# Performance work log

Measured on AMD Instinct MI355X. Metric: run time of the kernel, lower is better.

Reference implementation:

```python
import jax, jax.numpy as jnp
import numpy as np
import math

S, B, D = 2048, 8, 256
HEADS = 8
DPROJ = 128
DFF = 1024
DH = DPROJ // HEADS  # 16


def _layernorm(x, g, b, eps=1e-5):
    mu = jnp.mean(x, axis=-1, keepdims=True)
    var = jnp.mean((x - mu) ** 2, axis=-1, keepdims=True)
    return (x - mu) * jax.lax.rsqrt(var + eps) * g + b


def setup_inputs() -> dict:
    key = jax.random.key(0)
    ks = jax.random.split(key, 16)
    s = 0.02
    return {
        "src": jax.random.normal(ks[0], (S, B, D), dtype=jnp.float32),
        "Wq": jax.random.normal(ks[1], (D, DPROJ), dtype=jnp.float32) * s,
        "bq": jnp.zeros((DPROJ,), dtype=jnp.float32),
        "Wk": jax.random.normal(ks[2], (D, DPROJ), dtype=jnp.float32) * s,
        "bk": jnp.zeros((DPROJ,), dtype=jnp.float32),
        "Wv": jax.random.normal(ks[3], (D, DPROJ), dtype=jnp.float32) * s,
        "bv": jnp.zeros((DPROJ,), dtype=jnp.float32),
        "Wo": jax.random.normal(ks[4], (DPROJ, D), dtype=jnp.float32) * s,
        "ln1_g": jnp.ones((D,), dtype=jnp.float32),
        "ln1_b": jnp.zeros((D,), dtype=jnp.float32),
        "W1": jax.random.normal(ks[5], (D, DFF), dtype=jnp.float32) * s,
        "b1": jnp.zeros((DFF,), dtype=jnp.float32),
        "W2": jax.random.normal(ks[6], (DFF, D), dtype=jnp.float32) * s,
        "b2": jnp.zeros((D,), dtype=jnp.float32),
        "ln2_g": jnp.ones((D,), dtype=jnp.float32),
        "ln2_b": jnp.zeros((D,), dtype=jnp.float32),
    }


def reference(src, Wq, bq, Wk, bk, Wv, bv, Wo, ln1_g, ln1_b, W1, b1, W2, b2, ln2_g, ln2_b):
    # src: (S, B, D)
    q = src @ Wq + bq  # (S, B, DPROJ)
    k = src @ Wk + bk
    v = src @ Wv + bv

    # _reshape_to_batches: (S, B, h*dh) -> (S, B*h, dh), then sdpa moves batch first
    def split_heads(x):
        return jnp.transpose(x.reshape(S, B * HEADS, DH), (1, 0, 2))  # (B*h, S, dh)

    qh, kh, vh = split_heads(q), split_heads(k), split_heads(v)
    scores = jnp.einsum('bid,bjd->bij', qh, kh) / math.sqrt(DH)  # (B*h, S, S)
    attn = jax.nn.softmax(scores, axis=-1)
    ctx = jnp.einsum('bij,bjd->bid', attn, vh)  # (B*h, S, dh)

    # _reshape_from_batches: (B*h, S, dh) -> (S, B, DPROJ)
    ctx = jnp.transpose(ctx, (1, 0, 2)).reshape(S, B, DPROJ)
    y = ctx @ Wo  # (S, B, D), no bias

    x = _layernorm(src + y, ln1_g, ln1_b)
    ffn = jax.nn.relu(x @ W1 + b1) @ W2 + b2
    return _layernorm(x + ffn, ln2_g, ln2_b)
```

## Files before the change

### kernel.cpp

```cpp
#include <hip/hip_runtime.h>
#include <math.h>

#define SLEN 2048
#define BATCH 8
#define DMODEL 256
#define HEADS 8
#define DPROJ 128
#define DFF 1024
#define DH 16
#define MROWS (SLEN*BATCH)

typedef unsigned short u16;
typedef unsigned int u32;
typedef __attribute__((ext_vector_type(8))) short short8;
typedef __attribute__((ext_vector_type(4))) float f32x4;
typedef __attribute__((ext_vector_type(4))) unsigned short u16x4;

__device__ __forceinline__ u16 f2bf(float x) {
    union { float f; u32 u; } v; v.f = x;
    u32 r = v.u + 0x7FFFu + ((v.u >> 16) & 1u);
    return (u16)(r >> 16);
}
__device__ __forceinline__ float bf2f(u16 h) {
    union { u32 u; float f; } v; v.u = ((u32)h) << 16;
    return v.f;
}
__device__ __forceinline__ float fexp2(float x) { return __builtin_amdgcn_exp2f(x); }
__device__ __forceinline__ u32 pack_bf(float lo, float hi) {
    union { float f; u32 u; } a, b; a.f = lo; b.f = hi;
    return __builtin_amdgcn_perm(b.u, a.u, 0x07060302u);
}
__device__ __forceinline__ void gld16(const u16* g, u16* l) {
    __builtin_amdgcn_global_load_lds(
        (const __attribute__((address_space(1))) void*)g,
        (__attribute__((address_space(3))) void*)l, 16, 0, 0);
}

__global__ void prep_kernel(const float* __restrict__ src, u16* __restrict__ srcb,
                            const float* __restrict__ Wq, const float* __restrict__ Wk,
                            const float* __restrict__ Wv, const float* __restrict__ Wo,
                            const float* __restrict__ W1, const float* __restrict__ W2,
                            u16* __restrict__ WqT, u16* __restrict__ WkT,
                            u16* __restrict__ WvT, u16* __restrict__ WoT,
                            u16* __restrict__ W1T, u16* __restrict__ W2T) {
    if (blockIdx.x < 4096) {
        int idx = (blockIdx.x * 256 + threadIdx.x) * 4;
        float4 v = *(const float4*)(src + idx);
        u16x4 o;
        o.x = f2bf(v.x); o.y = f2bf(v.y); o.z = f2bf(v.z); o.w = f2bf(v.w);
        *(u16x4*)(srcb + idx) = o;
        return;
    }
    int i = (blockIdx.x - 4096) * 256 + threadIdx.x;
    if (i < 32768) {
        int n = i >> 8, k = i & 255;
        WqT[i] = f2bf(Wq[k * 128 + n]);
    } else if (i < 65536) {
        int j = i - 32768; int n = j >> 8, k = j & 255;
        WkT[j] = f2bf(Wk[k * 128 + n]);
    } else if (i < 98304) {
        int j = i - 65536; int n = j >> 8, k = j & 255;
        WvT[j] = f2bf(Wv[k * 128 + n]);
    } else if (i < 131072) {
        int j = i - 98304; int n = j >> 7, k = j & 127;
        WoT[j] = f2bf(Wo[k * 256 + n]);
    } else if (i < 393216) {
        int j = i - 131072; int n = j >> 8, k = j & 255;
        W1T[j] = f2bf(W1[k * 1024 + n]);
    } else if (i < 655360) {
        int j = i - 393216; int n = j >> 10, k = j & 1023;
        W2T[j] = f2bf(W2[k * 256 + n]);
    }
}

template<int BM, int BN, bool RELU, bool HAS_BIAS, bool OUT_BF16>
__global__ void mfma_gemm(const u16* __restrict__ A, const u16* __restrict__ BT,
                          const float* __restrict__ bias, void* __restrict__ Cout,
                          int M, int N, int K) {
    constexpr int MI = BM / 32;
    constexpr int NJ = BN / 32;
    __shared__ __align__(16) u16 As[2][BM * 32];
    __shared__ __align__(16) u16 Bs[2][BN * 32];
    const int tid = threadIdx.x;
    const int row0 = blockIdx.x * BM;
    const int col0 = blockIdx.y * BN;
    const int w = tid >> 6, l = tid & 63;
    const int wr = (w & 1) * (BM / 2), wc = (w >> 1) * (BN / 2);
    const int lcol = l & 15, lrow = (l >> 4) * 4, g = l >> 4;
    const int sl = l >> 2;
    const int swc = ((l & 3) ^ (sl & 3)) * 8;
    const int fsw = (g ^ (lcol & 3)) * 8;

    const u16* Ag0 = A + (size_t)(row0 + 16 * w + sl) * K + swc;
    const u16* Bg0 = BT + (size_t)(col0 + 16 * w + sl) * K + swc;
    const int lofs = (16 * w) * 32;

    f32x4 acc[MI][NJ] = {};
    gld16(Ag0, As[0] + lofs);
    if (BM == 128) gld16(Ag0 + (size_t)64 * K, As[0] + lofs + 64 * 32);
    gld16(Bg0, Bs[0] + lofs);
    if (BN == 128) gld16(Bg0 + (size_t)64 * K, Bs[0] + lofs + 64 * 32);
    __syncthreads();

    int cur = 0;
    for (int k0 = 0; k0 < K; k0 += 32) {
        if (k0 + 32 < K) {
            const int nb = cur ^ 1;
            gld16(Ag0 + k0 + 32, As[nb] + lofs);
            if (BM == 128) gld16(Ag0 + (size_t)64 * K + k0 + 32, As[nb] + lofs + 64 * 32);
            gld16(Bg0 + k0 + 32, Bs[nb] + lofs);
            if (BN == 128) gld16(Bg0 + (size_t)64 * K + k0 + 32, Bs[nb] + lofs + 64 * 32);
        }
        short8 af[MI], bf[NJ];
        #pragma unroll
        for (int i = 0; i < MI; ++i)
            af[i] = *(const short8*)(As[cur] + (wr + i * 16 + lcol) * 32 + fsw);
        #pragma unroll
        for (int j = 0; j < NJ; ++j)
            bf[j] = *(const short8*)(Bs[cur] + (wc + j * 16 + lcol) * 32 + fsw);
        #pragma unroll
        for (int i = 0; i < MI; ++i)
            #pragma unroll
            for (int j = 0; j < NJ; ++j)
                acc[i][j] = __builtin_amdgcn_mfma_f32_16x16x32_bf16(
                    af[i], bf[j], acc[i][j], 0, 0, 0);
        __syncthreads();
        cur ^= 1;
    }
    float bv[NJ];
    #pragma unroll
    for (int j = 0; j < NJ; ++j)
        bv[j] = HAS_BIAS ? bias[col0 + wc + j * 16 + lcol] : 0.f;
    #pragma unroll
    for (int i = 0; i < MI; ++i) {
        #pragma unroll
        for (int r = 0; r < 4; ++r) {
            size_t grow = row0 + wr + i * 16 + lrow + r;
            #pragma unroll
            for (int j = 0; j < NJ; ++j) {
                int gcol = col0 + wc + j * 16 + lcol;
                float c = acc[i][j][r] + bv[j];
                if (RELU) c = fmaxf(c, 0.f);
                if (OUT_BF16) ((u16*)Cout)[grow * N + gcol] = f2bf(c);
                else          ((float*)Cout)[grow * N + gcol] = c;
            }
        }
    }
}

__global__ void qkv_mfma(const u16* __restrict__ A,
                         const u16* __restrict__ WqT, const u16* __restrict__ WkT,
                         const u16* __restrict__ WvT,
                         const float* __restrict__ bq, const float* __restrict__ bk,
                         const float* __restrict__ bv,
                         u16* __restrict__ qhp, u16* __restrict__ khp,
                         u16* __restrict__ vhb) {
    const int which = blockIdx.z;
    const u16* BT   = which == 0 ? WqT : (which == 1 ? WkT : WvT);
    const float* bs = which == 0 ? bq : (which == 1 ? bk : bv);
    const float scale = which == 0 ? 0.25f * 1.44269504f : 1.0f;
    __shared__ __align__(16) u16 As[2][128 * 32];
    __shared__ __align__(16) u16 Bs[2][128 * 32];
    const int tid = threadIdx.x;
    const int row0 = blockIdx.x * 128;
    const int w = tid >> 6, l = tid & 63;
    const int wr = (w & 1) * 64, wc = (w >> 1) * 64;
    const int lcol = l & 15, lrow = (l >> 4) * 4, g = l >> 4;
    const int sl = l >> 2;
    const int swc = ((l & 3) ^ (sl & 3)) * 8;
    const int fsw = (g ^ (lcol & 3)) * 8;

    const u16* Ag0 = A + (size_t)(row0 + 16 * w + sl) * DMODEL + swc;
    const u16* Bg0 = BT + (size_t)(16 * w + sl) * DMODEL + swc;
    const int lofs = (16 * w) * 32;

    f32x4 acc[4][4] = {};
    gld16(Ag0, As[0] + lofs);
    gld16(Ag0 + (size_t)64 * DMODEL, As[0] + lofs + 64 * 32);
    gld16(Bg0, Bs[0] + lofs);
    gld16(Bg0 + (size_t)64 * DMODEL, Bs[0] + lofs + 64 * 32);
    __syncthreads();

    int cur = 0;
    for (int k0 = 0; k0 < DMODEL; k0 += 32) {
        if (k0 + 32 < DMODEL) {
            const int nb = cur ^ 1;
            gld16(Ag0 + k0 + 32, As[nb] + lofs);
            gld16(Ag0 + (size_t)64 * DMODEL + k0 + 32, As[nb] + lofs + 64 * 32);
            gld16(Bg0 + k0 + 32, Bs[nb] + lofs);
            gld16(Bg0 + (size_t)64 * DMODEL + k0 + 32, Bs[nb] + lofs + 64 * 32);
        }
        short8 af[4], bf[4];
        #pragma unroll
        for (int i = 0; i < 4; ++i)
            af[i] = *(const short8*)(As[cur] + (wr + i * 16 + lcol) * 32 + fsw);
        #pragma unroll
        for (int j = 0; j < 4; ++j)
            bf[j] = *(const short8*)(Bs[cur] + (wc + j * 16 + lcol) * 32 + fsw);
        #pragma unroll
        for (int i = 0; i < 4; ++i)
            #pragma unroll
            for (int j = 0; j < 4; ++j)
                acc[i][j] = __builtin_amdgcn_mfma_f32_16x16x32_bf16(
                    af[i], bf[j], acc[i][j], 0, 0, 0);
        __syncthreads();
        cur ^= 1;
    }
    #pragma unroll
    for (int i = 0; i < 4; ++i) {
        #pragma unroll
        for (int r = 0; r < 4; ++r) {
            int grow = row0 + wr + i * 16 + lrow + r;
            int b = grow & 7, s = grow >> 3;
            #pragma unroll
            for (int j = 0; j < 4; ++j) {
                int gcol = wc + j * 16 + lcol;
                int h = gcol >> 4, d = gcol & 15;
                float c = acc[i][j][r] + bs[gcol];
                if (which == 2) {
                    vhb[((size_t)(b * 8 + h) * SLEN + s) * 16 + d] = f2bf(c);
                } else {
                    u16* base = (which == 0 ? qhp : khp)
                              + ((size_t)(b * 8 + h) * SLEN + s) * 32;
                    base[d] = f2bf(c * scale);
                    base[d + 16] = 0;
                }
            }
        }
    }
}

__global__ void transpose_v(const u16* __restrict__ vhb, u16* __restrict__ vT) {
    __shared__ u16 T[128 * 24];
    const int bh = blockIdx.y;
    const int c0 = blockIdx.x * 128;
    const int t = threadIdx.x;
    {
        int key = t >> 1, half = t & 1;
        *(uint4*)(T + key * 24 + half * 8) =
            *(const uint4*)(vhb + ((size_t)bh * SLEN + c0 + key) * 16 + half * 8);
    }
    __syncthreads();
    int d = t >> 4, k8 = (t & 15) * 8;
    u16x4 o0, o1;
    o0.x = T[(k8 + 0) * 24 + d]; o0.y = T[(k8 + 1) * 24 + d];
    o0.z = T[(k8 + 2) * 24 + d]; o0.w = T[(k8 + 3) * 24 + d];
    o1.x = T[(k8 + 4) * 24 + d]; o1.y = T[(k8 + 5) * 24 + d];
    o1.z = T[(k8 + 6) * 24 + d]; o1.w = T[(k8 + 7) * 24 + d];
    u16* dst = vT + ((size_t)bh * 16 + d) * SLEN + c0 + k8;
    *(u16x4*)dst = o0;
    *(u16x4*)(dst + 4) = o1;
}

__global__ __launch_bounds__(256, 4)
void attn_mfma(const u16* __restrict__ qg, const u16* __restrict__ kg,
               const u16* __restrict__ vT, u16* __restrict__ ctx) {
    __shared__ __align__(16) u16 Ks[2][2][64 * 32];
    __shared__ __align__(16) u16 Vs[2][2][16 * 64];
    const int bh = blockIdx.y;
    const int q0 = blockIdx.x * 128;
    const int tid = threadIdx.x;
    const int w = tid >> 6, l = tid & 63;
    const int qc = l & 15, g = l >> 4;

    short8 qf[2];
    {
        const u16* qbase = qg + ((size_t)bh * SLEN + q0 + w * 32) * 32;
        qf[0] = *(const short8*)(qbase + qc * 32 + 8 * g);
        qf[1] = *(const short8*)(qbase + (16 + qc) * 32 + 8 * g);
    }

    const int sl = l >> 2;
    const int swc = ((l & 3) ^ (sl & 3)) * 8;
    const u16* Kg = kg + (size_t)bh * SLEN * 32 + (size_t)(16 * w + sl) * 32 + swc;
    u16* KsF = (u16*)Ks;
    u16* lK = KsF + (16 * w) * 32;
    const int vr = l >> 3, vc = l & 7;
    const int vsw0 = (vc ^ (vr & 7)) * 8;
    const u16* Vg0 = vT + ((size_t)bh * 16 + vr) * SLEN + vsw0;
    const u16* Vg1 = vT + ((size_t)bh * 16 + 8 + vr) * SLEN + vsw0;
    u16* VsF = (u16*)Vs;
    const int fsw = (g ^ (qc & 3)) * 8;
    const int qx = qc & 7, gh = g >> 1, gs = (g & 1) * 4;
    const int vrow = qc * 64;

    f32x4 o_[2] = {};
    f32x4 ls[2] = {};
    const short one_bf = (short)0x3F80;
    short8 onesB = {one_bf, one_bf, one_bf, one_bf, one_bf, one_bf, one_bf, one_bf};

    auto compute_tile = [&](const u16* Kc, const u16* Vc) {
        short8 kf[4];
        #pragma unroll
        for (int kj = 0; kj < 4; ++kj)
            kf[kj] = *(const short8*)(Kc + (kj * 16 + qc) * 32 + fsw);
        short8 vfrag[2];
        #pragma unroll
        for (int ks = 0; ks < 2; ++ks) {
            union { u32 d[4]; short8 v; } vv;
            uint2 va = *(const uint2*)(Vc + vrow + ((4 * ks + gh) ^ qx) * 8 + gs);
            uint2 vb = *(const uint2*)(Vc + vrow + ((4 * ks + 2 + gh) ^ qx) * 8 + gs);
            vv.d[0] = va.x; vv.d[1] = va.y; vv.d[2] = vb.x; vv.d[3] = vb.y;
            vfrag[ks] = vv.v;
        }
        f32x4 s_[4][2];
        #pragma unroll
        for (int kj = 0; kj < 4; ++kj)
            #pragma unroll
            for (int mi = 0; mi < 2; ++mi) {
                f32x4 zz = {0.f, 0.f, 0.f, 0.f};
                s_[kj][mi] = __builtin_amdgcn_mfma_f32_16x16x32_bf16(
                    kf[kj], qf[mi], zz, 0, 0, 0);
            }
        u32 dd[2][4][2];
        #pragma unroll
        for (int mi = 0; mi < 2; ++mi)
            #pragma unroll
            for (int kj = 0; kj < 4; ++kj) {
                f32x4 sv = s_[kj][mi];
                dd[mi][kj][0] = pack_bf(fexp2(sv[0]), fexp2(sv[1]));
                dd[mi][kj][1] = pack_bf(fexp2(sv[2]), fexp2(sv[3]));
            }
        #pragma unroll
        for (int ks = 0; ks < 2; ++ks)
            #pragma unroll
            for (int mi = 0; mi < 2; ++mi) {
                union { u32 d[4]; short8 v; } ap;
                ap.d[0] = dd[mi][2 * ks][0];     ap.d[1] = dd[mi][2 * ks][1];
                ap.d[2] = dd[mi][2 * ks + 1][0]; ap.d[3] = dd[mi][2 * ks + 1][1];
                o_[mi] = __builtin_amdgcn_mfma_f32_16x16x32_bf16(ap.v, vfrag[ks], o_[mi], 0, 0, 0);
                ls[mi] = __builtin_amdgcn_mfma_f32_16x16x32_bf16(ap.v, onesB, ls[mi], 0, 0, 0);
            }
    };

    gld16(Kg,                 lK);
    gld16(Kg + 2048,          lK + 2048);
    if (w == 0) { gld16(Vg0,      VsF);        gld16(Vg0 + 64,  VsF + 1024); }
    if (w == 1) { gld16(Vg1,      VsF + 512);  gld16(Vg1 + 64,  VsF + 1536); }
    __syncthreads();

    int cur = 0;
    for (int pt = 0; pt < 16; ++pt) {
        if (pt + 1 < 16) {
            const size_t ko = (size_t)(pt + 1) * 2 * 2048;
            const int    vo = (pt + 1) * 128;
            const int nb = cur ^ 1;
            gld16(Kg + ko,        KsF + nb * 4096 + (16 * w) * 32);
            gld16(Kg + ko + 2048, KsF + nb * 4096 + 2048 + (16 * w) * 32);
            if (w == 0) {
                gld16(Vg0 + vo,      VsF + nb * 2048);
                gld16(Vg0 + vo + 64, VsF + nb * 2048 + 1024);
            }
            if (w == 1) {
                gld16(Vg1 + vo,      VsF + nb * 2048 + 512);
                gld16(Vg1 + vo + 64, VsF + nb * 2048 + 1536);
            }
        }
        compute_tile(KsF + cur * 4096,        VsF + cur * 2048);
        compute_tile(KsF + cur * 4096 + 2048, VsF + cur * 2048 + 1024);
        __syncthreads();
        cur ^= 1;
    }

    const int b = bh >> 3, h = bh & 7;
    #pragma unroll
    for (int mi = 0; mi < 2; ++mi)
        #pragma unroll
        for (int r = 0; r < 4; ++r) {
            int qrow = q0 + w * 32 + mi * 16 + 4 * g + r;
            ctx[((size_t)qrow * BATCH + b) * DPROJ + h * DH + qc] =
                f2bf(o_[mi][r] / ls[mi][r]);
        }
}

__global__ void ln1_kernel(const float* __restrict__ src, const u16* __restrict__ y,
                           const float* __restrict__ g, const float* __restrict__ bb,
                           u16* __restrict__ xb) {
    const int w = threadIdx.x >> 6, l = threadIdx.x & 63;
    const int row = blockIdx.x * 4 + w;
    const int c = l * 4;
    size_t base = (size_t)row * DMODEL;
    float4 s4 = *(const float4*)(src + base + c);
    u16x4 y4 = *(const u16x4*)(y + base + c);
    float v[4] = { s4.x + bf2f(y4.x), s4.y + bf2f(y4.y),
                   s4.z + bf2f(y4.z), s4.w + bf2f(y4.w) };
    float sum = v[0] + v[1] + v[2] + v[3];
    float ss  = v[0]*v[0] + v[1]*v[1] + v[2]*v[2] + v[3]*v[3];
    #pragma unroll
    for (int off = 1; off < 64; off <<= 1) {
        sum += __shfl_xor(sum, off);
        ss  += __shfl_xor(ss, off);
    }
    float mu = sum * (1.0f / 256.0f);
    float var = ss * (1.0f / 256.0f) - mu * mu;
    float rs = rsqrtf(var + 1e-5f);
    float4 g4 = *(const float4*)(g + c);
    float4 b4 = *(const float4*)(bb + c);
    u16x4 o;
    o.x = f2bf((v[0] - mu) * rs * g4.x + b4.x);
    o.y = f2bf((v[1] - mu) * rs * g4.y + b4.y);
    o.z = f2bf((v[2] - mu) * rs * g4.z + b4.z);
    o.w = f2bf((v[3] - mu) * rs * g4.w + b4.w);
    *(u16x4*)(xb + base + c) = o;
}

__global__ void ln2_kernel(const u16* __restrict__ x, const u16* __restrict__ f,
                           const float* __restrict__ g, const float* __restrict__ bb,
                           float* __restrict__ out) {
    const int w = threadIdx.x >> 6, l = threadIdx.x & 63;
    const int row = blockIdx.x * 4 + w;
    const int c = l * 4;
    size_t base = (size_t)row * DMODEL;
    u16x4 x4 = *(const u16x4*)(x + base + c);
    u16x4 f4 = *(const u16x4*)(f + base + c);
    float v[4] = { bf2f(x4.x) + bf2f(f4.x), bf2f(x4.y) + bf2f(f4.y),
                   bf2f(x4.z) + bf2f(f4.z), bf2f(x4.w) + bf2f(f4.w) };
    float sum = v[0] + v[1] + v[2] + v[3];
    float ss  = v[0]*v[0] + v[1]*v[1] + v[2]*v[2] + v[3]*v[3];
    #pragma unroll
    for (int off = 1; off < 64; off <<= 1) {
        sum += __shfl_xor(sum, off);
        ss  += __shfl_xor(ss, off);
    }
    float mu = sum * (1.0f / 256.0f);
    float var = ss * (1.0f / 256.0f) - mu * mu;
    float rs = rsqrtf(var + 1e-5f);
    float4 g4 = *(const float4*)(g + c);
    float4 b4 = *(const float4*)(bb + c);
    float4 o;
    o.x = (v[0] - mu) * rs * g4.x + b4.x;
    o.y = (v[1] - mu) * rs * g4.y + b4.y;
    o.z = (v[2] - mu) * rs * g4.z + b4.z;
    o.w = (v[3] - mu) * rs * g4.w + b4.w;
    *(float4*)(out + base + c) = o;
}

extern "C" void kernel_launch(void* const* d_in, const int* in_sizes, int n_in,
                              void* d_out, int out_size, void* d_ws, size_t ws_size,
                              hipStream_t stream) {
    const float* src = (const float*)d_in[0];
    const float* Wq  = (const float*)d_in[1];
    const float* bq  = (const float*)d_in[2];
    const float* Wk  = (const float*)d_in[3];
    const float* bk  = (const float*)d_in[4];
    const float* Wv  = (const float*)d_in[5];
    const float* bv  = (const float*)d_in[6];
    const float* Wo  = (const float*)d_in[7];
    const float* g1  = (const float*)d_in[8];
    const float* be1 = (const float*)d_in[9];
    const float* W1  = (const float*)d_in[10];
    const float* b1  = (const float*)d_in[11];
    const float* W2  = (const float*)d_in[12];
    const float* b2  = (const float*)d_in[13];
    const float* g2  = (const float*)d_in[14];
    const float* be2 = (const float*)d_in[15];
    char* ws = (char*)d_ws;
    float* out = (float*)d_out;

    u16* qhp  = (u16*)(ws + 0);
    u16* khp  = (u16*)(ws + 8388608);
    u16* vhb  = (u16*)(ws + 16777216);
    u16* vT   = (u16*)(ws + 20971520);
    u16* ctxb = (u16*)(ws + 25165824);
    u16* yb   = (u16*)(ws + 29360128);
    u16* hb   = (u16*)(ws + 0);
    u16* xb   = (u16*)(ws + 37748736);
    u16* fb   = (u16*)(ws + 46137344);
    u16* srcb = (u16*)(ws + 54525952);
    u16* WqT  = (u16*)(ws + 62914560);
    u16* WkT  = (u16*)(ws + 62980096);
    u16* WvT  = (u16*)(ws + 63045632);
    u16* WoT  = (u16*)(ws + 63111168);
    u16* W1T  = (u16*)(ws + 63176704);
    u16* W2T  = (u16*)(ws + 63700992);

    prep_kernel<<<6656, 256, 0, stream>>>(src, srcb, Wq, Wk, Wv, Wo, W1, W2,
                                          WqT, WkT, WvT, WoT, W1T, W2T);
    qkv_mfma<<<dim3(128, 1, 3), 256, 0, stream>>>(srcb, WqT, WkT, WvT,
                                                  bq, bk, bv, qhp, khp, vhb);
    transpose_v<<<dim3(16, 64), 256, 0, stream>>>(vhb, vT);
    attn_mfma<<<dim3(16, 64), 256, 0, stream>>>(qhp, khp, vT, ctxb);
    mfma_gemm<64, 64, false, false, true><<<dim3(256, 4), 256, 0, stream>>>(
        ctxb, WoT, nullptr, yb, MROWS, DMODEL, DPROJ);
    ln1_kernel<<<MROWS / 4, 256, 0, stream>>>(src, yb, g1, be1, xb);
    mfma_gemm<128, 128, true, true, true><<<dim3(128, 8), 256, 0, stream>>>(
        xb, W1T, b1, hb, MROWS, DFF, DMODEL);
    mfma_gemm<64, 64, false, true, true><<<dim3(256, 4), 256, 0, stream>>>(
        hb, W2T, b2, fb, MROWS, DMODEL, DFF);
    ln2_kernel<<<MROWS / 4, 256, 0, stream>>>(xb, fb, g2, be2, out);
}
```

Before: 209.4 us.

## Fuse output projections with residual add and LayerNorm in full-row GEMM kernel

Adds a gemm_ln kernel in which each block computes a 32-row by 256-column tile, covering the full model width. Bias, residual add and LayerNorm are applied in the epilogue, with row statistics reduced by shuffles and a small shared buffer. It replaces the Wo GEMM plus ln1 and the W2 GEMM plus ln2, removing two launches and the bf16 round trips of y and the FFN output. In exchange the grid shrinks to 512 blocks, each doing more work per block, and the small tiles re-read the weight matrix many times, which could hurt the K=1024 GEMM.

```diff
diff --git a/kernel.cpp b/kernel.cpp
--- a/kernel.cpp
+++ b/kernel.cpp
@@ -144,6 +144,113 @@
                 if (OUT_BF16) ((u16*)Cout)[grow * N + gcol] = f2bf(c);
                 else          ((float*)Cout)[grow * N + gcol] = c;
             }
+        }
+    }
+}
+
+template<bool HAS_BIAS, bool RESID_F32, bool OUT_BF16>
+__global__ void gemm_ln(const u16* __restrict__ A, const u16* __restrict__ BT,
+                        const float* __restrict__ bias,
+                        const void* __restrict__ resid,
+                        const float* __restrict__ lng, const float* __restrict__ lnb,
+                        void* __restrict__ Cout, int K) {
+    __shared__ __align__(16) u16 As[2][32 * 32];
+    __shared__ __align__(16) u16 Bs[2][256 * 32];
+    __shared__ float Ls[2][32][2];
+    const int tid = threadIdx.x;
+    const int row0 = blockIdx.x * 32;
+    const int w = tid >> 6, l = tid & 63;
+    const int wr = (w & 1) * 16, wc = (w >> 1) * 128;
+    const int lcol = l & 15, lrow = (l >> 4) * 4, g = l >> 4;
+    const int sl = l >> 2;
+    const int swc = ((l & 3) ^ (sl & 3)) * 8;
+    const int fsw = (g ^ (lcol & 3)) * 8;
+
+    const u16* Ag = A + (size_t)(row0 + 16 * (w & 1) + sl) * K + swc;
+    u16* lA = (u16*)As + (16 * (w & 1)) * 32;
+    const u16* Bg[4];
+    u16* lB[4];
+    #pragma unroll
+    for (int t = 0; t < 4; ++t) {
+        Bg[t] = BT + (size_t)(16 * (w + 4 * t) + sl) * K + swc;
+        lB[t] = (u16*)Bs + (16 * (w + 4 * t)) * 32;
+    }
+
+    f32x4 acc[8] = {};
+    if (w < 2) gld16(Ag, lA);
+    #pragma unroll
+    for (int t = 0; t < 4; ++t) gld16(Bg[t], lB[t]);
+    __syncthreads();
+
+    int cur = 0;
+    for (int k0 = 0; k0 < K; k0 += 32) {
+        if (k0 + 32 < K) {
+            const int nb = cur ^ 1;
+            if (w < 2) gld16(Ag + k0 + 32, lA + nb * 1024);
+            #pragma unroll
+            for (int t = 0; t < 4; ++t) gld16(Bg[t] + k0 + 32, lB[t] + nb * 8192);
+        }
+        short8 af = *(const short8*)((u16*)As + cur * 1024 + (wr + lcol) * 32 + fsw);
+        short8 bf[8];
+        #pragma unroll
+        for (int j = 0; j < 8; ++j)
+            bf[j] = *(const short8*)((u16*)Bs + cur * 8192 + (wc + j * 16 + lcol) * 32 + fsw);
+        #pragma unroll
+        for (int j = 0; j < 8; ++j)
+            acc[j] = __builtin_amdgcn_mfma_f32_16x16x32_bf16(af, bf[j], acc[j], 0, 0, 0);
+        __syncthreads();
+        cur ^= 1;
+    }
+
+    #pragma unroll
+    for (int j = 0; j < 8; ++j) {
+        const int col = wc + j * 16 + lcol;
+        const float bv = HAS_BIAS ? bias[col] : 0.f;
+        #pragma unroll
+        for (int r = 0; r < 4; ++r) {
+            const size_t row = (size_t)row0 + wr + lrow + r;
+            float rv;
+            if (RESID_F32) rv = ((const float*)resid)[row * 256 + col];
+            else           rv = bf2f(((const u16*)resid)[row * 256 + col]);
+            acc[j][r] += bv + rv;
+        }
+    }
+    float s[4] = {0.f, 0.f, 0.f, 0.f}, q[4] = {0.f, 0.f, 0.f, 0.f};
+    #pragma unroll
+    for (int j = 0; j < 8; ++j)
+        #pragma unroll
+        for (int r = 0; r < 4; ++r) { s[r] += acc[j][r]; q[r] += acc[j][r] * acc[j][r]; }
+    #pragma unroll
+    for (int off = 1; off < 16; off <<= 1)
+        #pragma unroll
+        for (int r = 0; r < 4; ++r) { s[r] += __shfl_xor(s[r], off); q[r] += __shfl_xor(q[r], off); }
+    if (lcol == 0)
+        #pragma unroll
+        for (int r = 0; r < 4; ++r) {
+            Ls[w >> 1][wr + lrow + r][0] = s[r];
+            Ls[w >> 1][wr + lrow + r][1] = q[r];
+        }
+    __syncthreads();
+    float mu[4], rs[4];
+    #pragma unroll
+    for (int r = 0; r < 4; ++r) {
+        const int row = wr + lrow + r;
+        const float fs = Ls[0][row][0] + Ls[1][row][0];
+        const float fq = Ls[0][row][1] + Ls[1][row][1];
+        mu[r] = fs * (1.0f / 256.0f);
+        const float var = fq * (1.0f / 256.0f) - mu[r] * mu[r];
+        rs[r] = rsqrtf(var + 1e-5f);
+    }
+    #pragma unroll
+    for (int j = 0; j < 8; ++j) {
+        const int col = wc + j * 16 + lcol;
+        const float gv = lng[col], b2v = lnb[col];
+        #pragma unroll
+        for (int r = 0; r < 4; ++r) {
+            const size_t row = (size_t)row0 + wr + lrow + r;
+            const float o = (acc[j][r] - mu[r]) * rs[r] * gv + b2v;
+            if (OUT_BF16) ((u16*)Cout)[row * 256 + col] = f2bf(o);
+            else          ((float*)Cout)[row * 256 + col] = o;
         }
     }
 }
@@ -373,68 +480,6 @@
         }
 }
 
-__global__ void ln1_kernel(const float* __restrict__ src, const u16* __restrict__ y,
-                           const float* __restrict__ g, const float* __restrict__ bb,
-                           u16* __restrict__ xb) {
-    const int w = threadIdx.x >> 6, l = threadIdx.x & 63;
-    const int row = blockIdx.x * 4 + w;
-    const int c = l * 4;
-    size_t base = (size_t)row * DMODEL;
-    float4 s4 = *(const float4*)(src + base + c);
-    u16x4 y4 = *(const u16x4*)(y + base + c);
-    float v[4] = { s4.x + bf2f(y4.x), s4.y + bf2f(y4.y),
-                   s4.z + bf2f(y4.z), s4.w + bf2f(y4.w) };
-    float sum = v[0] + v[1] + v[2] + v[3];
-    float ss  = v[0]*v[0] + v[1]*v[1] + v[2]*v[2] + v[3]*v[3];
-    #pragma unroll
-    for (int off = 1; off < 64; off <<= 1) {
-        sum += __shfl_xor(sum, off);
-        ss  += __shfl_xor(ss, off);
-    }
-    float mu = sum * (1.0f / 256.0f);
-    float var = ss * (1.0f / 256.0f) - mu * mu;
-    float rs = rsqrtf(var + 1e-5f);
-    float4 g4 = *(const float4*)(g + c);
-    float4 b4 = *(const float4*)(bb + c);
-    u16x4 o;
-    o.x = f2bf((v[0] - mu) * rs * g4.x + b4.x);
-    o.y = f2bf((v[1] - mu) * rs * g4.y + b4.y);
-    o.z = f2bf((v[2] - mu) * rs * g4.z + b4.z);
-    o.w = f2bf((v[3] - mu) * rs * g4.w + b4.w);
-    *(u16x4*)(xb + base + c) = o;
-}
-
-__global__ void ln2_kernel(const u16* __restrict__ x, const u16* __restrict__ f,
-                           const float* __restrict__ g, const float* __restrict__ bb,
-                           float* __restrict__ out) {
-    const int w = threadIdx.x >> 6, l = threadIdx.x & 63;
-    const int row = blockIdx.x * 4 + w;
-    const int c = l * 4;
-    size_t base = (size_t)row * DMODEL;
-    u16x4 x4 = *(const u16x4*)(x + base + c);
-    u16x4 f4 = *(const u16x4*)(f + base + c);
-    float v[4] = { bf2f(x4.x) + bf2f(f4.x), bf2f(x4.y) + bf2f(f4.y),
-                   bf2f(x4.z) + bf2f(f4.z), bf2f(x4.w) + bf2f(f4.w) };
-    float sum = v[0] + v[1] + v[2] + v[3];
-    float ss  = v[0]*v[0] + v[1]*v[1] + v[2]*v[2] + v[3]*v[3];
-    #pragma unroll
-    for (int off = 1; off < 64; off <<= 1) {
-        sum += __shfl_xor(sum, off);
-        ss  += __shfl_xor(ss, off);
-    }
-    float mu = sum * (1.0f / 256.0f);
-    float var = ss * (1.0f / 256.0f) - mu * mu;
-    float rs = rsqrtf(var + 1e-5f);
-    float4 g4 = *(const float4*)(g + c);
-    float4 b4 = *(const float4*)(bb + c);
-    float4 o;
-    o.x = (v[0] - mu) * rs * g4.x + b4.x;
-    o.y = (v[1] - mu) * rs * g4.y + b4.y;
-    o.z = (v[2] - mu) * rs * g4.z + b4.z;
-    o.w = (v[3] - mu) * rs * g4.w + b4.w;
-    *(float4*)(out + base + c) = o;
-}
-
 extern "C" void kernel_launch(void* const* d_in, const int* in_sizes, int n_in,
                               void* d_out, int out_size, void* d_ws, size_t ws_size,
                               hipStream_t stream) {
@@ -462,10 +507,8 @@
     u16* vhb  = (u16*)(ws + 16777216);
     u16* vT   = (u16*)(ws + 20971520);
     u16* ctxb = (u16*)(ws + 25165824);
-    u16* yb   = (u16*)(ws + 29360128);
     u16* hb   = (u16*)(ws + 0);
     u16* xb   = (u16*)(ws + 37748736);
-    u16* fb   = (u16*)(ws + 46137344);
     u16* srcb = (u16*)(ws + 54525952);
     u16* WqT  = (u16*)(ws + 62914560);
     u16* WkT  = (u16*)(ws + 62980096);
@@ -480,12 +523,10 @@
                                                   bq, bk, bv, qhp, khp, vhb);
     transpose_v<<<dim3(16, 64), 256, 0, stream>>>(vhb, vT);
     attn_mfma<<<dim3(16, 64), 256, 0, stream>>>(qhp, khp, vT, ctxb);
-    mfma_gemm<64, 64, false, false, true><<<dim3(256, 4), 256, 0, stream>>>(
-        ctxb, WoT, nullptr, yb, MROWS, DMODEL, DPROJ);
-    ln1_kernel<<<MROWS / 4, 256, 0, stream>>>(src, yb, g1, be1, xb);
+    gemm_ln<false, true, true><<<512, 256, 0, stream>>>(
+        ctxb, WoT, nullptr, src, g1, be1, xb, DPROJ);
     mfma_gemm<128, 128, true, true, true><<<dim3(128, 8), 256, 0, stream>>>(
         xb, W1T, b1, hb, MROWS, DFF, DMODEL);
-    mfma_gemm<64, 64, false, true, true><<<dim3(256, 4), 256, 0, stream>>>(
-        hb, W2T, b2, fb, MROWS, DMODEL, DFF);
-    ln2_kernel<<<MROWS / 4, 256, 0, stream>>>(xb, fb, g2, be2, out);
-}
+    gemm_ln<true, false, false><<<512, 256, 0, stream>>>(
+        hb, W2T, b2, xb, g2, be2, out, DFF);
+}
```

Result: no change. 208.4 us (-0.5%).
